# Kernel tuning notes

Hardware: AMD Instinct MI355X
Metric: run time of the kernel (lower is better)

Reference implementation:

```python
import jax, jax.numpy as jnp
import numpy as np

D_MODEL = 1024
N_HEADS = 16


def setup_inputs() -> dict:
    key = jax.random.key(0)
    ks = jax.random.split(key, 5)
    sigma = (1.0 / D_MODEL) ** 0.5
    return {
        "x": jax.random.normal(ks[0], (4, 2048, D_MODEL), dtype=jnp.float32),
        "W_q": jax.random.normal(ks[1], (D_MODEL, D_MODEL), dtype=jnp.float32) * sigma,
        "W_k": jax.random.normal(ks[2], (D_MODEL, D_MODEL), dtype=jnp.float32) * sigma,
        "W_v": jax.random.normal(ks[3], (D_MODEL, D_MODEL), dtype=jnp.float32) * sigma,
        "W_o": jax.random.normal(ks[4], (D_MODEL, D_MODEL), dtype=jnp.float32) * sigma,
    }


def reference(x, W_q, W_k, W_v, W_o):
    b, s, d = x.shape
    h = N_HEADS
    d_h = d // h
    # Projections: original does einsum('d_out dim, ... dim -> ... d_out') == x @ W.T
    def proj(W):
        y = jnp.einsum('bsd,ed->bse', x, W)
        # ... seq (head d_h) -> ... head seq d_h
        return y.reshape(b, s, h, d_h).transpose(0, 2, 1, 3)
    Q, K, V = proj(W_q), proj(W_k), proj(W_v)
    scale = 1.0 / jnp.sqrt(jnp.asarray(d_h, dtype=x.dtype))
    scores = jnp.einsum('bhqd,bhkd->bhqk', Q, K) * scale  # [b,h,s,s]
    causal = jnp.tril(jnp.ones((s, s), dtype=bool))
    scores = jnp.where(causal, scores, -jnp.inf)
    attn = jax.nn.softmax(scores, axis=-1)
    out = jnp.einsum('bhqk,bhkd->bhqd', attn, V)  # [b,h,s,d_h]
    out = out.transpose(0, 2, 1, 3).reshape(b, s, d)
    # einsum(Temp, W_o, '... dim1, dim dim1 -> ... dim') == Temp @ W_o.T
    return jnp.einsum('bse,de->bsd', out, W_o)
```

## Files before the change

### kernel.cpp

```cpp
#include <hip/hip_runtime.h>

typedef __attribute__((ext_vector_type(8))) short s16x8;
typedef __attribute__((ext_vector_type(4))) float f32x4;
typedef unsigned short u16;
typedef unsigned int u32;
typedef unsigned long long u64;

__device__ __forceinline__ u16 f2bf(float f) {
  unsigned u = __builtin_bit_cast(unsigned, f);
  return (u16)((u + 0x7fffu + ((u >> 16) & 1u)) >> 16);
}

#define QSCALE 0.18033688011112042f
#define MFIX 16.0f

__device__ __forceinline__ void gld16(const u16* g, u16* l) {
  __builtin_amdgcn_global_load_lds(
      (const __attribute__((address_space(1))) void*)g,
      (__attribute__((address_space(3))) void*)l, 16, 0, 0);
}

__device__ __forceinline__ u32 pack_trunc(float a, float b) {
  return __builtin_amdgcn_perm(__builtin_bit_cast(u32, b),
                               __builtin_bit_cast(u32, a), 0x07060302u);
}

__global__ __launch_bounds__(256)
void cvt_bf16(const float* __restrict__ src, u16* __restrict__ dst, int n8)
{
  const int i = blockIdx.x * 256 + threadIdx.x;
  if (i < n8) {
    f32x4 a = ((const f32x4*)src)[2 * i];
    f32x4 b = ((const f32x4*)src)[2 * i + 1];
    s16x8 pk;
    pk[0] = (short)f2bf(a[0]); pk[1] = (short)f2bf(a[1]);
    pk[2] = (short)f2bf(a[2]); pk[3] = (short)f2bf(a[3]);
    pk[4] = (short)f2bf(b[0]); pk[5] = (short)f2bf(b[1]);
    pk[6] = (short)f2bf(b[2]); pk[7] = (short)f2bf(b[3]);
    ((s16x8*)dst)[i] = pk;
  }
}

__global__ __launch_bounds__(256)
void cvt_bf16_w(const float* __restrict__ s0, const float* __restrict__ s1,
                const float* __restrict__ s2, const float* __restrict__ s3,
                u16* __restrict__ d0, u16* __restrict__ d1,
                u16* __restrict__ d2, u16* __restrict__ d3)
{
  const int ws = blockIdx.y;
  const float* src = (ws == 0) ? s0 : (ws == 1) ? s1 : (ws == 2) ? s2 : s3;
  u16* dst = (ws == 0) ? d0 : (ws == 1) ? d1 : (ws == 2) ? d2 : d3;
  const int i = blockIdx.x * 256 + threadIdx.x;
  f32x4 a = ((const f32x4*)src)[2 * i];
  f32x4 b = ((const f32x4*)src)[2 * i + 1];
  s16x8 pk;
  pk[0] = (short)f2bf(a[0]); pk[1] = (short)f2bf(a[1]);
  pk[2] = (short)f2bf(a[2]); pk[3] = (short)f2bf(a[3]);
  pk[4] = (short)f2bf(b[0]); pk[5] = (short)f2bf(b[1]);
  pk[6] = (short)f2bf(b[2]); pk[7] = (short)f2bf(b[3]);
  ((s16x8*)dst)[i] = pk;
}

template<bool OUT_QKV>
__global__ __launch_bounds__(256)
void gemm97(const u16* __restrict__ A,
            const u16* __restrict__ B0, const u16* __restrict__ B1,
            const u16* __restrict__ B2,
            u16* __restrict__ o0, u16* __restrict__ o1, u16* __restrict__ o2,
            float* __restrict__ oF)
{
  const int by = blockIdx.x;
  const int bx = blockIdx.y;
  const int bz = blockIdx.z;
  const u16* B = (bz == 0) ? B0 : ((bz == 1) ? B1 : B2);
  u16* oQ = (bz == 0) ? o0 : ((bz == 1) ? o1 : o2);

  __shared__ u16 As[128 * 32];
  __shared__ u16 Bs[128 * 32];

  const int tid  = threadIdx.x;
  const int w    = tid >> 6;
  const int lane = tid & 63;
  const int quad = lane >> 4;
  const int l15  = lane & 15;
  const int wm   = (w >> 1) * 64;
  const int wn   = (w & 1) * 64;

  const int arb  = w * 32;
  const int srow = lane >> 2;
  const int scol = (lane & 3) * 8;
  const u16* ga = A + (size_t)(by * 128 + arb + srow) * 1024 + scol;
  const u16* gb = B + (size_t)(bx * 128 + arb + srow) * 1024 + scol;
  u16* la0 = &As[arb * 32];
  u16* la1 = &As[(arb + 16) * 32];
  u16* lb0 = &Bs[arb * 32];
  u16* lb1 = &Bs[(arb + 16) * 32];

  f32x4 acc[4][4];
  #pragma unroll
  for (int i = 0; i < 4; ++i)
    #pragma unroll
    for (int j = 0; j < 4; ++j)
      acc[i][j] = (f32x4){0.f, 0.f, 0.f, 0.f};

  for (int k0 = 0; k0 < 1024; k0 += 32) {
    gld16(ga + k0,               la0);
    gld16(ga + k0 + 16 * 1024,   la1);
    gld16(gb + k0,               lb0);
    gld16(gb + k0 + 16 * 1024,   lb1);
    __syncthreads();

    s16x8 af[4], bf[4];
    #pragma unroll
    for (int i = 0; i < 4; ++i)
      af[i] = *(const s16x8*)&As[(wm + i * 16 + l15) * 32 + quad * 8];
    #pragma unroll
    for (int i = 0; i < 4; ++i)
      bf[i] = *(const s16x8*)&Bs[(wn + i * 16 + l15) * 32 + quad * 8];
    #pragma unroll
    for (int mt = 0; mt < 4; ++mt)
      #pragma unroll
      for (int nt = 0; nt < 4; ++nt)
        acc[mt][nt] = __builtin_amdgcn_mfma_f32_16x16x32_bf16(
            af[mt], bf[nt], acc[mt][nt], 0, 0, 0);
    __syncthreads();
  }

  #pragma unroll
  for (int mt = 0; mt < 4; ++mt)
    #pragma unroll
    for (int nt = 0; nt < 4; ++nt)
      #pragma unroll
      for (int r = 0; r < 4; ++r) {
        const int row = by * 128 + wm + mt * 16 + quad * 4 + r;
        const int col = bx * 128 + wn + nt * 16 + l15;
        float v = acc[mt][nt][r];
        if (OUT_QKV) {
          if (bz == 0) v *= QSCALE;
          const int b = row >> 11, s = row & 2047, hh = col >> 6, d = col & 63;
          oQ[(size_t)(b * 16 + hh) * 131072 + s * 64 + d] = f2bf(v);
        } else {
          oF[(size_t)row * 1024 + col] = v;
        }
      }
}

__global__ __launch_bounds__(256)
void vtrans(const u16* __restrict__ Vb, u16* __restrict__ VT)
{
  const int st = blockIdx.x;
  const int bh = blockIdx.y;
  __shared__ u16 T[64 * 72];
  const int tid = threadIdx.x;
  const size_t base = (size_t)bh * 131072;
  #pragma unroll
  for (int p = 0; p < 2; ++p) {
    const int idx = tid + p * 256;
    const int row = idx >> 3;
    const int col = (idx & 7) * 8;
    s16x8 v = *(const s16x8*)(Vb + base + (size_t)(st * 64 + row) * 64 + col);
    #pragma unroll
    for (int e = 0; e < 8; ++e) T[(col + e) * 72 + row] = v[e];
  }
  __syncthreads();
  #pragma unroll
  for (int p = 0; p < 2; ++p) {
    const int idx = tid + p * 256;
    const int drow = idx >> 3;
    const int scol = (idx & 7) * 8;
    *(s16x8*)(VT + base + (size_t)drow * 2048 + st * 64 + scol) =
        *(const s16x8*)&T[drow * 72 + scol];
  }
}

#define LOADKV(jj)                                                             \
  do {                                                                         \
    _Pragma("unroll")                                                          \
    for (int p = 0; p < 2; ++p) {                                              \
      const int idx = tid + p * 256;                                           \
      const int key = idx >> 3, col = (idx & 7) * 8;                           \
      kreg[p] = *(const s16x8*)(Kg + base + (size_t)((jj) * 64 + key) * 64 + col); \
    }                                                                          \
    _Pragma("unroll")                                                          \
    for (int p = 0; p < 2; ++p) {                                              \
      const int idx = tid + p * 256;                                           \
      const int d = idx >> 3, col = (idx & 7) * 8;                             \
      vreg[p] = *(const s16x8*)(VTg + base + (size_t)d * 2048 + (jj) * 64 + col); \
    }                                                                          \
  } while (0)

#define STOREKV()                                                              \
  do {                                                                         \
    _Pragma("unroll")                                                          \
    for (int p = 0; p < 2; ++p) {                                              \
      const int idx = tid + p * 256;                                           \
      const int key = idx >> 3, col = (idx & 7) * 8;                           \
      const int slot = (key & 3) * 16 + (key >> 2);                            \
      *(s16x8*)&Ks[slot * 72 + col] = kreg[p];                                 \
    }                                                                          \
    _Pragma("unroll")                                                          \
    for (int p = 0; p < 2; ++p) {                                              \
      const int idx = tid + p * 256;                                           \
      const int d = idx >> 3, col = (idx & 7) * 8;                             \
      *(s16x8*)&Vt[d * 72 + col] = vreg[p];                                    \
    }                                                                          \
  } while (0)

#define ATTN_STEP(t, Pw, qtt)                                                  \
  do {                                                                         \
    f32x4 S[4];                                                                \
    __builtin_amdgcn_s_setprio(1);                                             \
    _Pragma("unroll")                                                          \
    for (int nt = 0; nt < 4; ++nt) {                                           \
      s16x8 b0 = *(const s16x8*)&Ks[(nt * 16 + l15) * 72 + quad * 8];          \
      s16x8 b1 = *(const s16x8*)&Ks[(nt * 16 + l15) * 72 + 32 + quad * 8];     \
      f32x4 z = (f32x4){-MFIX, -MFIX, -MFIX, -MFIX};                           \
      z = __builtin_amdgcn_mfma_f32_16x16x32_bf16(aq[t][0], b0, z, 0, 0, 0);   \
      z = __builtin_amdgcn_mfma_f32_16x16x32_bf16(aq[t][1], b1, z, 0, 0, 0);   \
      S[nt] = z;                                                               \
    }                                                                          \
    __builtin_amdgcn_s_setprio(0);                                             \
    if (j == (qtt)) {                                                          \
      _Pragma("unroll")                                                        \
      for (int nt = 0; nt < 4; ++nt)                                           \
        _Pragma("unroll")                                                      \
        for (int r = 0; r < 4; ++r) {                                          \
          const int kg = 4 * l15 + nt;                                         \
          const int qg = w * 16 + quad * 4 + r;                                \
          if (kg > qg) S[nt][r] = -1e30f;                                      \
        }                                                                      \
    }                                                                          \
    _Pragma("unroll")                                                          \
    for (int r = 0; r < 4; ++r) {                                              \
      const float p0 = __builtin_amdgcn_exp2f(S[0][r]);                        \
      const float p1 = __builtin_amdgcn_exp2f(S[1][r]);                        \
      const float p2 = __builtin_amdgcn_exp2f(S[2][r]);                        \
      const float p3 = __builtin_amdgcn_exp2f(S[3][r]);                        \
      const u64 pk = (u64)pack_trunc(p0, p1) |                                 \
                     ((u64)pack_trunc(p2, p3) << 32);                          \
      *(u64*)&(Pw)[(quad * 4 + r) * 72 + 4 * l15] = pk;                        \
    }                                                                          \
    s16x8 a0 = *(const s16x8*)&(Pw)[l15 * 72 + quad * 8];                      \
    s16x8 a1 = *(const s16x8*)&(Pw)[l15 * 72 + 32 + quad * 8];                 \
    __builtin_amdgcn_s_setprio(1);                                             \
    liacc[t] = __builtin_amdgcn_mfma_f32_16x16x32_bf16(a0, ones, liacc[t], 0, 0, 0); \
    liacc[t] = __builtin_amdgcn_mfma_f32_16x16x32_bf16(a1, ones, liacc[t], 0, 0, 0); \
    _Pragma("unroll")                                                          \
    for (int dt = 0; dt < 4; ++dt) {                                           \
      s16x8 b0 = *(const s16x8*)&Vt[(dt * 16 + l15) * 72 + quad * 8];          \
      s16x8 b1 = *(const s16x8*)&Vt[(dt * 16 + l15) * 72 + 32 + quad * 8];     \
      O[t][dt] = __builtin_amdgcn_mfma_f32_16x16x32_bf16(a0, b0, O[t][dt], 0, 0, 0); \
      O[t][dt] = __builtin_amdgcn_mfma_f32_16x16x32_bf16(a1, b1, O[t][dt], 0, 0, 0); \
    }                                                                          \
    __builtin_amdgcn_s_setprio(0);                                             \
  } while (0)

__global__ __launch_bounds__(256, 4)
void attn_kernel(const u16* __restrict__ Qg, const u16* __restrict__ Kg,
                 const u16* __restrict__ VTg, u16* __restrict__ out)
{
  const int bh = blockIdx.x;
  const int pi = blockIdx.y;
  const int b = bh >> 4, h = bh & 15;
  const int qt0 = 31 - pi;
  const int qt1 = pi;

  __shared__ u16 Qs[128 * 72];
  __shared__ u16 Ks[64 * 72];
  __shared__ u16 Vt[64 * 72];

  const int tid = threadIdx.x;
  const int w = tid >> 6, lane = tid & 63, quad = lane >> 4, l15 = lane & 15;
  const size_t base = (size_t)bh * 131072;

  {
    const int col = (tid & 7) * 8;
    #pragma unroll
    for (int p = 0; p < 4; ++p) {
      const int row = (tid >> 3) + p * 32;
      const int gq = (row < 64) ? (qt0 * 64 + row) : (qt1 * 64 + (row - 64));
      *(s16x8*)&Qs[row * 72 + col] =
          *(const s16x8*)(Qg + base + (size_t)gq * 64 + col);
    }
  }

  s16x8 kreg[2], vreg[2];
  LOADKV(0);
  __syncthreads();

  s16x8 aq[2][2];
  #pragma unroll
  for (int t = 0; t < 2; ++t)
    #pragma unroll
    for (int ks = 0; ks < 2; ++ks)
      aq[t][ks] = *(const s16x8*)&Qs[(t * 64 + w * 16 + l15) * 72 + ks * 32 + quad * 8];

  u16* Pw0 = &Qs[(w * 16) * 72];
  u16* Pw1 = &Qs[(64 + w * 16) * 72];

  s16x8 ones;
  #pragma unroll
  for (int e = 0; e < 8; ++e) ones[e] = (short)0x3F80;

  f32x4 O[2][4], liacc[2];
  #pragma unroll
  for (int t = 0; t < 2; ++t) {
    #pragma unroll
    for (int dt = 0; dt < 4; ++dt) O[t][dt] = (f32x4){0.f, 0.f, 0.f, 0.f};
    liacc[t] = (f32x4){0.f, 0.f, 0.f, 0.f};
  }

  STOREKV();
  __syncthreads();

  for (int j = 0; j <= qt0; ++j) {
    if (j < qt0) LOADKV(j + 1);
    ATTN_STEP(0, Pw0, qt0);
    if (j <= qt1) ATTN_STEP(1, Pw1, qt1);
    __syncthreads();
    if (j < qt0) {
      STOREKV();
      __syncthreads();
    }
  }

  #pragma unroll
  for (int t = 0; t < 2; ++t) {
    const int qtt = t ? qt1 : qt0;
    #pragma unroll
    for (int r = 0; r < 4; ++r) {
      const float inv = __builtin_amdgcn_rcpf(liacc[t][r]);
      const int sq = qtt * 64 + w * 16 + quad * 4 + r;
      #pragma unroll
      for (int dt = 0; dt < 4; ++dt)
        out[(size_t)(b * 2048 + sq) * 1024 + h * 64 + dt * 16 + l15] =
            f2bf(O[t][dt][r] * inv);
    }
  }
}

extern "C" void kernel_launch(void* const* d_in, const int* in_sizes, int n_in,
                              void* d_out, int out_size, void* d_ws, size_t ws_size,
                              hipStream_t stream) {
  (void)in_sizes; (void)n_in; (void)out_size; (void)ws_size;
  const float* x  = (const float*)d_in[0];
  const float* Wq = (const float*)d_in[1];
  const float* Wk = (const float*)d_in[2];
  const float* Wv = (const float*)d_in[3];
  const float* Wo = (const float*)d_in[4];
  float* out = (float*)d_out;

  u16* W16 = (u16*)d_ws;
  u16* xb  = W16;
  u16* VT  = W16;
  u16* Qb  = W16 + 8388608;
  u16* Kb  = W16 + 16777216;
  u16* Vb  = W16 + 25165824;
  u16* AO  = Vb;
  u16* Wqb = W16 + 33554432;
  u16* Wkb = Wqb + 1048576;
  u16* Wvb = Wkb + 1048576;
  u16* Wob = Wvb + 1048576;

  dim3 blk(256);
  cvt_bf16<<<dim3(4096), blk, 0, stream>>>(x,  xb,  1048576);
  cvt_bf16_w<<<dim3(512, 4), blk, 0, stream>>>(Wq, Wk, Wv, Wo,
                                               Wqb, Wkb, Wvb, Wob);

  gemm97<true ><<<dim3(64, 8, 3), blk, 0, stream>>>(
      xb, Wqb, Wkb, Wvb, Qb, Kb, Vb, nullptr);
  vtrans<<<dim3(32, 64), blk, 0, stream>>>(Vb, VT);
  attn_kernel<<<dim3(64, 16), blk, 0, stream>>>(Qb, Kb, VT, AO);
  gemm97<false><<<dim3(64, 8, 1), blk, 0, stream>>>(
      AO, Wob, Wob, Wob, nullptr, nullptr, nullptr, out);
}
```

Before: 272.6 us.

## Split paired causal query tiles into one tile per attention block

The attention kernel previously paired query tiles (31-pi, pi) in each block so every block did equal causal work and reused each loaded K/V tile for two query tiles. Now each block handles a single 64-row query tile, the grid grows to 32 tiles per head, Q is loaded straight into registers instead of through shared memory, and a smaller LDS footprint allows the launch bound to rise to 5 blocks per CU. The aim is more parallelism and occupancy. In exchange, each K/V tile is loaded once per query tile rather than once per pair, and block runtimes become unbalanced, with heavy tiles scheduled first.

```diff
diff --git a/kernel.cpp b/kernel.cpp
--- a/kernel.cpp
+++ b/kernel.cpp
@@ -206,136 +206,111 @@
     }                                                                          \
   } while (0)
 
-#define ATTN_STEP(t, Pw, qtt)                                                  \
-  do {                                                                         \
-    f32x4 S[4];                                                                \
-    __builtin_amdgcn_s_setprio(1);                                             \
-    _Pragma("unroll")                                                          \
-    for (int nt = 0; nt < 4; ++nt) {                                           \
-      s16x8 b0 = *(const s16x8*)&Ks[(nt * 16 + l15) * 72 + quad * 8];          \
-      s16x8 b1 = *(const s16x8*)&Ks[(nt * 16 + l15) * 72 + 32 + quad * 8];     \
-      f32x4 z = (f32x4){-MFIX, -MFIX, -MFIX, -MFIX};                           \
-      z = __builtin_amdgcn_mfma_f32_16x16x32_bf16(aq[t][0], b0, z, 0, 0, 0);   \
-      z = __builtin_amdgcn_mfma_f32_16x16x32_bf16(aq[t][1], b1, z, 0, 0, 0);   \
-      S[nt] = z;                                                               \
-    }                                                                          \
-    __builtin_amdgcn_s_setprio(0);                                             \
-    if (j == (qtt)) {                                                          \
-      _Pragma("unroll")                                                        \
-      for (int nt = 0; nt < 4; ++nt)                                           \
-        _Pragma("unroll")                                                      \
-        for (int r = 0; r < 4; ++r) {                                          \
-          const int kg = 4 * l15 + nt;                                         \
-          const int qg = w * 16 + quad * 4 + r;                                \
-          if (kg > qg) S[nt][r] = -1e30f;                                      \
-        }                                                                      \
-    }                                                                          \
-    _Pragma("unroll")                                                          \
-    for (int r = 0; r < 4; ++r) {                                              \
-      const float p0 = __builtin_amdgcn_exp2f(S[0][r]);                        \
-      const float p1 = __builtin_amdgcn_exp2f(S[1][r]);                        \
-      const float p2 = __builtin_amdgcn_exp2f(S[2][r]);                        \
-      const float p3 = __builtin_amdgcn_exp2f(S[3][r]);                        \
-      const u64 pk = (u64)pack_trunc(p0, p1) |                                 \
-                     ((u64)pack_trunc(p2, p3) << 32);                          \
-      *(u64*)&(Pw)[(quad * 4 + r) * 72 + 4 * l15] = pk;                        \
-    }                                                                          \
-    s16x8 a0 = *(const s16x8*)&(Pw)[l15 * 72 + quad * 8];                      \
-    s16x8 a1 = *(const s16x8*)&(Pw)[l15 * 72 + 32 + quad * 8];                 \
-    __builtin_amdgcn_s_setprio(1);                                             \
-    liacc[t] = __builtin_amdgcn_mfma_f32_16x16x32_bf16(a0, ones, liacc[t], 0, 0, 0); \
-    liacc[t] = __builtin_amdgcn_mfma_f32_16x16x32_bf16(a1, ones, liacc[t], 0, 0, 0); \
-    _Pragma("unroll")                                                          \
-    for (int dt = 0; dt < 4; ++dt) {                                           \
-      s16x8 b0 = *(const s16x8*)&Vt[(dt * 16 + l15) * 72 + quad * 8];          \
-      s16x8 b1 = *(const s16x8*)&Vt[(dt * 16 + l15) * 72 + 32 + quad * 8];     \
-      O[t][dt] = __builtin_amdgcn_mfma_f32_16x16x32_bf16(a0, b0, O[t][dt], 0, 0, 0); \
-      O[t][dt] = __builtin_amdgcn_mfma_f32_16x16x32_bf16(a1, b1, O[t][dt], 0, 0, 0); \
-    }                                                                          \
-    __builtin_amdgcn_s_setprio(0);                                             \
-  } while (0)
-
-__global__ __launch_bounds__(256, 4)
+__global__ __launch_bounds__(256, 5)
 void attn_kernel(const u16* __restrict__ Qg, const u16* __restrict__ Kg,
                  const u16* __restrict__ VTg, u16* __restrict__ out)
 {
   const int bh = blockIdx.x;
-  const int pi = blockIdx.y;
+  const int qt = 31 - blockIdx.y;
   const int b = bh >> 4, h = bh & 15;
-  const int qt0 = 31 - pi;
-  const int qt1 = pi;
-
-  __shared__ u16 Qs[128 * 72];
+
   __shared__ u16 Ks[64 * 72];
   __shared__ u16 Vt[64 * 72];
+  __shared__ u16 Ps[64 * 72];
 
   const int tid = threadIdx.x;
   const int w = tid >> 6, lane = tid & 63, quad = lane >> 4, l15 = lane & 15;
   const size_t base = (size_t)bh * 131072;
 
-  {
-    const int col = (tid & 7) * 8;
-    #pragma unroll
-    for (int p = 0; p < 4; ++p) {
-      const int row = (tid >> 3) + p * 32;
-      const int gq = (row < 64) ? (qt0 * 64 + row) : (qt1 * 64 + (row - 64));
-      *(s16x8*)&Qs[row * 72 + col] =
-          *(const s16x8*)(Qg + base + (size_t)gq * 64 + col);
-    }
-  }
+  s16x8 aq[2];
+  #pragma unroll
+  for (int ks = 0; ks < 2; ++ks)
+    aq[ks] = *(const s16x8*)(Qg + base +
+        (size_t)(qt * 64 + w * 16 + l15) * 64 + ks * 32 + quad * 8);
+
+  u16* Pw = &Ps[(w * 16) * 72];
+
+  s16x8 ones;
+  #pragma unroll
+  for (int e = 0; e < 8; ++e) ones[e] = (short)0x3F80;
+
+  f32x4 O[4], liacc;
+  #pragma unroll
+  for (int dt = 0; dt < 4; ++dt) O[dt] = (f32x4){0.f, 0.f, 0.f, 0.f};
+  liacc = (f32x4){0.f, 0.f, 0.f, 0.f};
 
   s16x8 kreg[2], vreg[2];
   LOADKV(0);
-  __syncthreads();
-
-  s16x8 aq[2][2];
-  #pragma unroll
-  for (int t = 0; t < 2; ++t)
-    #pragma unroll
-    for (int ks = 0; ks < 2; ++ks)
-      aq[t][ks] = *(const s16x8*)&Qs[(t * 64 + w * 16 + l15) * 72 + ks * 32 + quad * 8];
-
-  u16* Pw0 = &Qs[(w * 16) * 72];
-  u16* Pw1 = &Qs[(64 + w * 16) * 72];
-
-  s16x8 ones;
-  #pragma unroll
-  for (int e = 0; e < 8; ++e) ones[e] = (short)0x3F80;
-
-  f32x4 O[2][4], liacc[2];
-  #pragma unroll
-  for (int t = 0; t < 2; ++t) {
-    #pragma unroll
-    for (int dt = 0; dt < 4; ++dt) O[t][dt] = (f32x4){0.f, 0.f, 0.f, 0.f};
-    liacc[t] = (f32x4){0.f, 0.f, 0.f, 0.f};
-  }
-
   STOREKV();
   __syncthreads();
 
-  for (int j = 0; j <= qt0; ++j) {
-    if (j < qt0) LOADKV(j + 1);
-    ATTN_STEP(0, Pw0, qt0);
-    if (j <= qt1) ATTN_STEP(1, Pw1, qt1);
+  for (int j = 0; j <= qt; ++j) {
+    if (j < qt) LOADKV(j + 1);
+
+    f32x4 S[4];
+    __builtin_amdgcn_s_setprio(1);
+    #pragma unroll
+    for (int nt = 0; nt < 4; ++nt) {
+      s16x8 b0 = *(const s16x8*)&Ks[(nt * 16 + l15) * 72 + quad * 8];
+      s16x8 b1 = *(const s16x8*)&Ks[(nt * 16 + l15) * 72 + 32 + quad * 8];
+      f32x4 z = (f32x4){-MFIX, -MFIX, -MFIX, -MFIX};
+      z = __builtin_amdgcn_mfma_f32_16x16x32_bf16(aq[0], b0, z, 0, 0, 0);
+      z = __builtin_amdgcn_mfma_f32_16x16x32_bf16(aq[1], b1, z, 0, 0, 0);
+      S[nt] = z;
+    }
+    __builtin_amdgcn_s_setprio(0);
+
+    if (j == qt) {
+      #pragma unroll
+      for (int nt = 0; nt < 4; ++nt)
+        #pragma unroll
+        for (int r = 0; r < 4; ++r) {
+          const int kg = 4 * l15 + nt;
+          const int qg = w * 16 + quad * 4 + r;
+          if (kg > qg) S[nt][r] = -1e30f;
+        }
+    }
+
+    #pragma unroll
+    for (int r = 0; r < 4; ++r) {
+      const float p0 = __builtin_amdgcn_exp2f(S[0][r]);
+      const float p1 = __builtin_amdgcn_exp2f(S[1][r]);
+      const float p2 = __builtin_amdgcn_exp2f(S[2][r]);
+      const float p3 = __builtin_amdgcn_exp2f(S[3][r]);
+      const u64 pk = (u64)pack_trunc(p0, p1) |
+                     ((u64)pack_trunc(p2, p3) << 32);
+      *(u64*)&Pw[(quad * 4 + r) * 72 + 4 * l15] = pk;
+    }
+    s16x8 a0 = *(const s16x8*)&Pw[l15 * 72 + quad * 8];
+    s16x8 a1 = *(const s16x8*)&Pw[l15 * 72 + 32 + quad * 8];
+
+    __builtin_amdgcn_s_setprio(1);
+    liacc = __builtin_amdgcn_mfma_f32_16x16x32_bf16(a0, ones, liacc, 0, 0, 0);
+    liacc = __builtin_amdgcn_mfma_f32_16x16x32_bf16(a1, ones, liacc, 0, 0, 0);
+    #pragma unroll
+    for (int dt = 0; dt < 4; ++dt) {
+      s16x8 b0 = *(const s16x8*)&Vt[(dt * 16 + l15) * 72 + quad * 8];
+      s16x8 b1 = *(const s16x8*)&Vt[(dt * 16 + l15) * 72 + 32 + quad * 8];
+      O[dt] = __builtin_amdgcn_mfma_f32_16x16x32_bf16(a0, b0, O[dt], 0, 0, 0);
+      O[dt] = __builtin_amdgcn_mfma_f32_16x16x32_bf16(a1, b1, O[dt], 0, 0, 0);
+    }
+    __builtin_amdgcn_s_setprio(0);
+
     __syncthreads();
-    if (j < qt0) {
+    if (j < qt) {
       STOREKV();
       __syncthreads();
     }
   }
 
   #pragma unroll
-  for (int t = 0; t < 2; ++t) {
-    const int qtt = t ? qt1 : qt0;
-    #pragma unroll
-    for (int r = 0; r < 4; ++r) {
-      const float inv = __builtin_amdgcn_rcpf(liacc[t][r]);
-      const int sq = qtt * 64 + w * 16 + quad * 4 + r;
-      #pragma unroll
-      for (int dt = 0; dt < 4; ++dt)
-        out[(size_t)(b * 2048 + sq) * 1024 + h * 64 + dt * 16 + l15] =
-            f2bf(O[t][dt][r] * inv);
-    }
+  for (int r = 0; r < 4; ++r) {
+    const float inv = __builtin_amdgcn_rcpf(liacc[r]);
+    const int sq = qt * 64 + w * 16 + quad * 4 + r;
+    #pragma unroll
+    for (int dt = 0; dt < 4; ++dt)
+      out[(size_t)(b * 2048 + sq) * 1024 + h * 64 + dt * 16 + l15] =
+          f2bf(O[dt][r] * inv);
   }
 }
 
@@ -370,7 +345,7 @@
   gemm97<true ><<<dim3(64, 8, 3), blk, 0, stream>>>(
       xb, Wqb, Wkb, Wvb, Qb, Kb, Vb, nullptr);
   vtrans<<<dim3(32, 64), blk, 0, stream>>>(Vb, VT);
-  attn_kernel<<<dim3(64, 16), blk, 0, stream>>>(Qb, Kb, VT, AO);
+  attn_kernel<<<dim3(64, 32), blk, 0, stream>>>(Qb, Kb, VT, AO);
   gemm97<false><<<dim3(64, 8, 1), blk, 0, stream>>>(
       AO, Wob, Wob, Wob, nullptr, nullptr, nullptr, out);
 }
```

Result: faster. 251.0 us (-7.9%).
